# Performance work log

Hardware: AMD Instinct MI355X
Metric: run time of the kernel (lower is better)

Reference implementation:

```python
import jax, jax.numpy as jnp
import numpy as np

N = 50000
E = 1600000
F_IN = 256
DIMS = 64
N_CLS = 16
R = 8


def glorot(key, shape):
    fan = shape[-2] + shape[-1] if len(shape) >= 2 else shape[-1] * 2
    std = jnp.sqrt(6.0 / fan)
    return jax.random.uniform(key, shape, jnp.float32, -std, std)


def setup_inputs() -> dict:
    key = jax.random.key(0)
    ks = jax.random.split(key, 12)
    x = jax.random.normal(ks[0], (N, F_IN), jnp.float32)
    edge_index = jax.random.randint(ks[1], (2, E), 0, N)
    edge_weight = jax.random.uniform(ks[2], (E,), jnp.float32)
    edge_color = jax.random.randint(ks[3], (E,), 0, R)
    W1 = glorot(ks[4], (R, F_IN, DIMS))
    atten1 = glorot(ks[5], (R, 2 * DIMS))
    root1 = glorot(ks[6], (F_IN, DIMS))
    bias1 = jnp.zeros((DIMS,), jnp.float32)
    W2 = glorot(ks[7], (R, DIMS, N_CLS))
    atten2 = glorot(ks[8], (R, 2 * N_CLS))
    root2 = glorot(ks[9], (DIMS, N_CLS))
    bias2 = jnp.zeros((N_CLS,), jnp.float32)
    return dict(x=x, edge_index=edge_index, edge_weight=edge_weight,
                edge_color=edge_color, W1=W1, atten1=atten1, root1=root1,
                bias1=bias1, W2=W2, atten2=atten2, root2=root2, bias2=bias2)


def wrgat_conv(x, src, dst, ew, ec, W, atten, root, bias):
    # x: [N, f_in]; W: [R, f_in, d]; atten: [R, 2d]
    d = W.shape[-1]
    xr = jnp.einsum('nf,rfd->rnd', x, W)            # [R, N, d] per-relation projection
    xi = xr[ec, dst]                                 # [E, d] dst (x_i)
    xj = xr[ec, src]                                 # [E, d] src (x_j)
    a_i = atten[:, :d][ec]                           # [E, d]
    a_j = atten[:, d:][ec]
    s = jnp.sum(a_i * xi + a_j * xj, axis=-1)        # [E]
    s = jax.nn.leaky_relu(s, 0.2)
    # segment softmax over (relation, destination) groups
    seg = ec * N + dst                               # [E], each edge belongs to one relation
    nseg = R * N
    m = jax.ops.segment_max(s, seg, num_segments=nseg)
    m = jnp.where(jnp.isfinite(m), m, 0.0)           # empty segments -> 0
    e = jnp.exp(s - m[seg])
    denom = jax.ops.segment_sum(e, seg, num_segments=nseg)
    alpha = e / jnp.maximum(denom[seg], 1e-16)
    msg = (alpha * ew)[:, None] * xj                 # [E, d]
    summed = jax.ops.segment_sum(msg, seg, num_segments=nseg).reshape(R, N, d)
    cnt = jax.ops.segment_sum(jnp.ones_like(ew), seg, num_segments=nseg).reshape(R, N, 1)
    out = (summed / jnp.maximum(cnt, 1.0)).sum(axis=0)  # mean aggr per relation, summed over relations
    return out + x @ root + bias


def reference(x, edge_index, edge_weight, edge_color, W1, atten1, root1, bias1,
              W2, atten2, root2, bias2):
    src, dst = edge_index[0], edge_index[1]          # PyG flow source_to_target: x_j=src, x_i=dst
    h = wrgat_conv(x, src, dst, edge_weight, edge_color, W1, atten1, root1, bias1)
    h = jax.nn.relu(h)                               # dropout p=0 -> identity
    h = wrgat_conv(h, src, dst, edge_weight, edge_color, W2, atten2, root2, bias2)
    return jax.nn.log_softmax(h, axis=1)
```

## Files before the change

### kernel.cpp

```cpp
#include <hip/hip_runtime.h>
#include <math.h>

#define N_NODES 50000
#define N_EDGES 1600000
#define F_IN    256
#define DIMS    64
#define N_CLS   16
#define R_REL   8
#define CAP     96

#define PROJ_BLKS 3519
#define CSR_BLKS  6250
#define FRONT_BLKS (PROJ_BLKS + CSR_BLKS)

typedef short bf16x8 __attribute__((ext_vector_type(8)));
typedef float f32x4  __attribute__((ext_vector_type(4)));
typedef unsigned int u32;
typedef const __attribute__((address_space(1))) u32* gas_ptr;
typedef __attribute__((address_space(3))) u32* las_ptr;

__device__ __forceinline__ void async16(const void* g, void* l) {
    __builtin_amdgcn_global_load_lds((gas_ptr)g, (las_ptr)l, 16, 0, 0);
}

__device__ __forceinline__ unsigned short f2bf(float f) {
    unsigned u = __float_as_uint(f);
    unsigned r = (u + 0x7fffu + ((u >> 16) & 1u)) >> 16;
    return (unsigned short)r;
}
__device__ __forceinline__ float bf2f(unsigned short u) {
    return __uint_as_float(((unsigned)u) << 16);
}

__device__ __forceinline__ void csr_edge(
        int e, const int* __restrict__ ei, const int* __restrict__ ecol,
        const float* __restrict__ ew, int* __restrict__ fill,
        u32* __restrict__ rec) {
    int s = ei[e], d = ei[N_EDGES + e], c = ecol[e];
    float w_ = ew[e];
    int ewq = (int)(w_ * 4096.f);
    if (ewq > 4095) ewq = 4095;
    int p = atomicAdd(&fill[d], 1);
    int idx = (p < CAP) ? d * CAP + p : N_NODES * CAP;
    u32 rv = ((u32)c << 29) | ((u32)s << 12) | (u32)ewq;
    __builtin_nontemporal_store(rv, &rec[idx]);
}

__global__ __launch_bounds__(256) void cvt_x_kernel(
        const float* __restrict__ x, ushort* __restrict__ xb) {
    int i4 = blockIdx.x * 256 + threadIdx.x;
    float4 v = ((const float4*)x)[i4];
    ushort4 o;
    o.x = f2bf(v.x); o.y = f2bf(v.y); o.z = f2bf(v.z); o.w = f2bf(v.w);
    ((ushort4*)xb)[i4] = o;
}

__global__ __launch_bounds__(256) void cvt_w_kernel(
        const float* __restrict__ W1, const float* __restrict__ root1,
        ushort* __restrict__ wt1) {
    int idx = blockIdx.x * 256 + threadIdx.x;
    int r = idx >> 14, rem = idx & 16383;
    int n = rem >> 8, k = rem & 255;
    float v = (r < 8) ? W1[((size_t)r * F_IN + k) * DIMS + n]
                      : root1[(size_t)k * DIMS + n];
    wt1[idx] = f2bf(v);
}

#define BM 128
__global__ __launch_bounds__(256, 6) void front_kernel(
        const ushort* __restrict__ xb, const ushort* __restrict__ wt1,
        const float* __restrict__ at1,
        ushort* __restrict__ xr1b, ushort* __restrict__ hrootb,
        float* __restrict__ si1, float* __restrict__ sj1,
        const int* __restrict__ ei, const int* __restrict__ ecol,
        const float* __restrict__ ew, int* __restrict__ fill,
        u32* __restrict__ rec) {
    __shared__ ushort xs[BM * 64];
    const int bid = blockIdx.x;
    const int t = threadIdx.x;

    int pb = -1, cb = -1;
    if (bid < 2 * PROJ_BLKS) { if (bid & 1) cb = bid >> 1; else pb = bid >> 1; }
    else cb = PROJ_BLKS + (bid - 2 * PROJ_BLKS);

    if (cb >= 0) {
        csr_edge(cb * 256 + t, ei, ecol, ew, fill, rec);
        return;
    }

    const int r = pb / 391;
    const int node0 = (pb % 391) * BM;
    const ushort* wrow = wt1 + (size_t)r * 64 * 256;

    const int w = t >> 6, lane = t & 63;
    const int lane15 = lane & 15, quad = lane >> 4;
    const int row0 = w * 32 + lane15;
    const int sw0 = row0 & 7;

    f32x4 acc[2][4];
    #pragma unroll
    for (int a = 0; a < 2; ++a)
        #pragma unroll
        for (int b = 0; b < 4; ++b)
            acc[a][b] = (f32x4){0.f, 0.f, 0.f, 0.f};

    for (int s = 0; s < 4; ++s) {
        __syncthreads();
        #pragma unroll
        for (int c = 0; c < 4; ++c) {
            int slot = c * 256 + t;
            int row = slot >> 3, k8p = slot & 7;
            int k8 = k8p ^ (row & 7);
            int node = node0 + row;
            if (node >= N_NODES) node = N_NODES - 1;
            async16(&xb[(size_t)node * 256 + s * 64 + k8 * 8],
                    &xs[(c * 256 + w * 64) * 8]);
        }
        __syncthreads();
        #pragma unroll
        for (int kk = 0; kk < 2; ++kk) {
            int k8 = kk * 4 + quad;
            int aidx = row0 * 64 + ((k8 ^ sw0) << 3);
            bf16x8 a0 = *(const bf16x8*)&xs[aidx];
            bf16x8 a1 = *(const bf16x8*)&xs[aidx + 16 * 64];
            int kg = s * 64 + kk * 32 + quad * 8;
            #pragma unroll
            for (int nt = 0; nt < 4; ++nt) {
                bf16x8 b = *(const bf16x8*)&wrow[(size_t)(nt * 16 + lane15) * 256 + kg];
                acc[0][nt] = __builtin_amdgcn_mfma_f32_16x16x32_bf16(a0, b, acc[0][nt], 0, 0, 0);
                acc[1][nt] = __builtin_amdgcn_mfma_f32_16x16x32_bf16(a1, b, acc[1][nt], 0, 0, 0);
            }
        }
    }

    const float* at = at1 + r * 128;
    #pragma unroll
    for (int mt = 0; mt < 2; ++mt) {
        float pi[4] = {0.f, 0.f, 0.f, 0.f};
        float pj[4] = {0.f, 0.f, 0.f, 0.f};
        #pragma unroll
        for (int nt = 0; nt < 4; ++nt) {
            int gcol = nt * 16 + lane15;
            float ai = 0.f, aj = 0.f;
            if (r < 8) { ai = at[gcol]; aj = at[64 + gcol]; }
            #pragma unroll
            for (int reg = 0; reg < 4; ++reg) {
                float v = acc[mt][nt][reg];
                int grow = node0 + w * 32 + mt * 16 + quad * 4 + reg;
                if (grow < N_NODES) {
                    if (r < 8)
                        xr1b[((size_t)r * N_NODES + grow) * 64 + gcol] = f2bf(v);
                    else
                        hrootb[(size_t)grow * 64 + gcol] = f2bf(v);
                }
                pi[reg] += ai * v;
                pj[reg] += aj * v;
            }
        }
        if (r < 8) {
            #pragma unroll
            for (int reg = 0; reg < 4; ++reg) {
                float s_ = pi[reg], u_ = pj[reg];
                #pragma unroll
                for (int off = 1; off < 16; off <<= 1) {
                    s_ += __shfl_xor(s_, off, 64);
                    u_ += __shfl_xor(u_, off, 64);
                }
                if (lane15 == 0) {
                    int grow = node0 + w * 32 + mt * 16 + quad * 4 + reg;
                    if (grow < N_NODES) {
                        si1[r * N_NODES + grow] = s_;
                        sj1[r * N_NODES + grow] = u_;
                    }
                }
            }
        }
    }
}

__global__ __launch_bounds__(256) void agg1s_kernel(
        const u32* __restrict__ rec, const int* __restrict__ fill,
        const float* __restrict__ si, const float* __restrict__ sj,
        const ushort* __restrict__ xr1b, const ushort* __restrict__ hrootb,
        const float* __restrict__ bias1, ushort* __restrict__ hb,
        const float* __restrict__ W2, const float* __restrict__ at2,
        ushort* __restrict__ xr2b, float* __restrict__ si2,
        float* __restrict__ sj2) {
    __shared__ u32   esrc2[4][CAP];
    __shared__ float ecoef2[4][CAP];
    __shared__ float hval[4][64];
    __shared__ float sden[4][8];
    __shared__ int   scnt[4][8];
    __shared__ int   ccur[4][8];
    __shared__ float ssi[4][8];
    const int t = threadIdx.x;
    const int w = t >> 6, lane = t & 63;
    const int d = blockIdx.x * 4 + w;
    if (lane < 8) {
        sden[w][lane] = 0.f; scnt[w][lane] = 0;
        ssi[w][lane] = si[lane * N_NODES + d];
    }
    const int n = min(fill[d], CAP);
    const int base = d * CAP;
    u32 pv[2] = {0, 0};
    #pragma unroll
    for (int ii = 0; ii < 2; ++ii) {
        int i = lane + ii * 64;
        if (i < n) {
            u32 rv = rec[base + i];
            pv[ii] = rv;
            atomicAdd(&scnt[w][rv >> 29], 1);
        }
    }
    if (lane == 0) {
        int o = 0;
        #pragma unroll
        for (int c = 0; c < 8; ++c) { ccur[w][c] = o; o += scnt[w][c]; }
    }
    #pragma unroll
    for (int ii = 0; ii < 2; ++ii) {
        int i = lane + ii * 64;
        if (i < n) {
            int pos = atomicAdd(&ccur[w][pv[ii] >> 29], 1);
            esrc2[w][pos] = pv[ii];
        }
    }
    float exv[2] = {0.f, 0.f};
    #pragma unroll
    for (int ii = 0; ii < 2; ++ii) {
        int i = lane + ii * 64;
        if (i < n) {
            u32 rv = esrc2[w][i];
            int c = rv >> 29, s = (rv >> 12) & 0x1FFFF;
            float sc = ssi[w][c] + sj[c * N_NODES + s];
            sc = sc > 0.f ? sc : 0.2f * sc;
            float e = __expf(sc);
            exv[ii] = e;
            atomicAdd(&sden[w][c], e);
        }
    }
    #pragma unroll
    for (int ii = 0; ii < 2; ++ii) {
        int i = lane + ii * 64;
        if (i < n) {
            u32 rv = esrc2[w][i];
            int c = rv >> 29;
            float ewf = ((float)(rv & 0xFFF) + 0.5f) * (1.f / 4096.f);
            ecoef2[w][i] = exv[ii] / fmaxf(sden[w][c], 1e-16f)
                           * ewf / (float)scnt[w][c];
        }
    }
    float a0 = 0.f, a1 = 0.f, a2 = 0.f, a3 = 0.f;
    int i = 0;
    for (; i + 4 <= n; i += 4) {
        u32 p0 = esrc2[w][i],     p1 = esrc2[w][i + 1];
        u32 p2 = esrc2[w][i + 2], p3 = esrc2[w][i + 3];
        float c0 = ecoef2[w][i],     c1 = ecoef2[w][i + 1];
        float c2 = ecoef2[w][i + 2], c3 = ecoef2[w][i + 3];
        int r0 = (p0 >> 29) * N_NODES + ((p0 >> 12) & 0x1FFFF);
        int r1 = (p1 >> 29) * N_NODES + ((p1 >> 12) & 0x1FFFF);
        int r2 = (p2 >> 29) * N_NODES + ((p2 >> 12) & 0x1FFFF);
        int r3 = (p3 >> 29) * N_NODES + ((p3 >> 12) & 0x1FFFF);
        a0 += c0 * bf2f(xr1b[(size_t)r0 * 64 + lane]);
        a1 += c1 * bf2f(xr1b[(size_t)r1 * 64 + lane]);
        a2 += c2 * bf2f(xr1b[(size_t)r2 * 64 + lane]);
        a3 += c3 * bf2f(xr1b[(size_t)r3 * 64 + lane]);
    }
    for (; i < n; ++i) {
        u32 p0 = esrc2[w][i];
        int r0 = (p0 >> 29) * N_NODES + ((p0 >> 12) & 0x1FFFF);
        a0 += ecoef2[w][i] * bf2f(xr1b[(size_t)r0 * 64 + lane]);
    }
    float hf = (a0 + a1) + (a2 + a3)
               + bf2f(hrootb[(size_t)d * 64 + lane]) + bias1[lane];
    hf = fmaxf(hf, 0.f);
    hb[(size_t)d * 64 + lane] = f2bf(hf);
    hval[w][lane] = hf;
    const int r_ = lane >> 4, c_ = lane & 15;
    float v0 = 0.f, v1 = 0.f;
    #pragma unroll 8
    for (int k = 0; k < 64; ++k) {
        float hk = hval[w][k];
        v0 += hk * W2[((size_t)r_ * 64 + k) * 16 + c_];
        v1 += hk * W2[((size_t)(r_ + 4) * 64 + k) * 16 + c_];
    }
    xr2b[((size_t)r_ * N_NODES + d) * 16 + c_] = f2bf(v0);
    xr2b[((size_t)(r_ + 4) * N_NODES + d) * 16 + c_] = f2bf(v1);
    float s0 = at2[r_ * 32 + c_] * v0,        j0 = at2[r_ * 32 + 16 + c_] * v0;
    float s1 = at2[(r_ + 4) * 32 + c_] * v1,  j1 = at2[(r_ + 4) * 32 + 16 + c_] * v1;
    #pragma unroll
    for (int off = 1; off < 16; off <<= 1) {
        s0 += __shfl_xor(s0, off, 64); j0 += __shfl_xor(j0, off, 64);
        s1 += __shfl_xor(s1, off, 64); j1 += __shfl_xor(j1, off, 64);
    }
    if (c_ == 0) {
        si2[r_ * N_NODES + d] = s0;       sj2[r_ * N_NODES + d] = j0;
        si2[(r_ + 4) * N_NODES + d] = s1; sj2[(r_ + 4) * N_NODES + d] = j1;
    }
}

__global__ __launch_bounds__(256) void agg2s_kernel(
        const u32* __restrict__ rec, const int* __restrict__ fill,
        const float* __restrict__ si, const float* __restrict__ sj,
        const ushort* __restrict__ xr2b, const ushort* __restrict__ hb,
        const float* __restrict__ root2, const float* __restrict__ bias2,
        float* __restrict__ out) {
    __shared__ float rsh[64][17];
    __shared__ float hsh[4][64];
    __shared__ u32   esrc2[4][CAP];
    __shared__ float ecoef2[4][CAP];
    __shared__ float sden[4][8];
    __shared__ int   scnt[4][8];
    __shared__ int   ccur[4][8];
    __shared__ float ssi[4][8];
    const int t = threadIdx.x;
    for (int i = t; i < DIMS * N_CLS; i += 256) rsh[i >> 4][i & 15] = root2[i];
    const int w = t >> 6, lane = t & 63;
    const int d = blockIdx.x * 4 + w;
    hsh[w][lane] = bf2f(hb[(size_t)d * 64 + lane]);
    if (lane < 8) {
        sden[w][lane] = 0.f; scnt[w][lane] = 0;
        ssi[w][lane] = si[lane * N_NODES + d];
    }
    const int n = min(fill[d], CAP);
    const int base = d * CAP;
    u32 pv[2] = {0, 0};
    #pragma unroll
    for (int ii = 0; ii < 2; ++ii) {
        int i = lane + ii * 64;
        if (i < n) {
            u32 rv = rec[base + i];
            pv[ii] = rv;
            atomicAdd(&scnt[w][rv >> 29], 1);
        }
    }
    if (lane == 0) {
        int o = 0;
        #pragma unroll
        for (int c = 0; c < 8; ++c) { ccur[w][c] = o; o += scnt[w][c]; }
    }
    #pragma unroll
    for (int ii = 0; ii < 2; ++ii) {
        int i = lane + ii * 64;
        if (i < n) {
            int pos = atomicAdd(&ccur[w][pv[ii] >> 29], 1);
            esrc2[w][pos] = pv[ii];
        }
    }
    float exv[2] = {0.f, 0.f};
    #pragma unroll
    for (int ii = 0; ii < 2; ++ii) {
        int i = lane + ii * 64;
        if (i < n) {
            u32 rv = esrc2[w][i];
            int c = rv >> 29, s = (rv >> 12) & 0x1FFFF;
            float sc = ssi[w][c] + sj[c * N_NODES + s];
            sc = sc > 0.f ? sc : 0.2f * sc;
            float e = __expf(sc);
            exv[ii] = e;
            atomicAdd(&sden[w][c], e);
        }
    }
    #pragma unroll
    for (int ii = 0; ii < 2; ++ii) {
        int i = lane + ii * 64;
        if (i < n) {
            u32 rv = esrc2[w][i];
            int c = rv >> 29;
            float ewf = ((float)(rv & 0xFFF) + 0.5f) * (1.f / 4096.f);
            ecoef2[w][i] = exv[ii] / fmaxf(sden[w][c], 1e-16f)
                           * ewf / (float)scnt[w][c];
        }
    }
    __syncthreads();
    const int sub = lane >> 4, cd = lane & 15;
    float acc = 0.f;
    for (int i = sub; i < n; i += 4) {
        u32 p = esrc2[w][i];
        int row = (p >> 29) * N_NODES + ((p >> 12) & 0x1FFFF);
        acc += ecoef2[w][i] * bf2f(xr2b[(size_t)row * 16 + cd]);
    }
    #pragma unroll
    for (int k0 = 0; k0 < 16; ++k0) {
        int k = sub * 16 + k0;
        acc += hsh[w][k] * rsh[k][cd];
    }
    acc += __shfl_xor(acc, 16, 64);
    acc += __shfl_xor(acc, 32, 64);
    if (sub == 0) {
        acc += bias2[cd];
        float m = acc;
        #pragma unroll
        for (int off = 8; off; off >>= 1) m = fmaxf(m, __shfl_xor(m, off, 16));
        float ex2 = expf(acc - m);
        float ssum = ex2;
        #pragma unroll
        for (int off = 8; off; off >>= 1) ssum += __shfl_xor(ssum, off, 16);
        out[(size_t)d * 16 + cd] = acc - m - logf(ssum);
    }
}

extern "C" void kernel_launch(void* const* d_in, const int* in_sizes, int n_in,
                              void* d_out, int out_size, void* d_ws, size_t ws_size,
                              hipStream_t stream) {
    const float* x     = (const float*)d_in[0];
    const int*   ei    = (const int*)  d_in[1];
    const float* ew    = (const float*)d_in[2];
    const int*   ecol  = (const int*)  d_in[3];
    const float* W1    = (const float*)d_in[4];
    const float* at1   = (const float*)d_in[5];
    const float* root1 = (const float*)d_in[6];
    const float* b1    = (const float*)d_in[7];
    const float* W2    = (const float*)d_in[8];
    const float* at2   = (const float*)d_in[9];
    const float* root2 = (const float*)d_in[10];
    const float* b2    = (const float*)d_in[11];
    float* out = (float*)d_out;
    float* ws  = (float*)d_ws;

    ushort*   xb    = (ushort*)(ws + 0);
    ushort*   wt1   = (ushort*)(ws + 6400000);
    ushort*   xr1b  = (ushort*)(ws + 6480000);
    ushort*   hrootb= (ushort*)(ws + 19280000);
    ushort*   xr2b  = (ushort*)(ws + 20880000);
    float*    si1   = ws + 24080000;
    float*    sj1   = ws + 24480000;
    float*    si2   = ws + 24880000;
    float*    sj2   = ws + 25280000;
    int*      fill  = (int*)(ws + 25680000);
    ushort*   hb    = (ushort*)(ws + 25730000);
    u32*      rec   = (u32*)(ws + 27330000);

    hipMemsetAsync(fill, 0, (size_t)N_NODES * 4, stream);

    cvt_x_kernel<<<12500, 256, 0, stream>>>(x, xb);
    cvt_w_kernel<<<576, 256, 0, stream>>>(W1, root1, wt1);
    front_kernel<<<FRONT_BLKS, 256, 0, stream>>>(xb, wt1, at1, xr1b, hrootb,
                                                 si1, sj1, ei, ecol, ew, fill, rec);
    agg1s_kernel<<<12500, 256, 0, stream>>>(rec, fill, si1, sj1, xr1b, hrootb,
                                            b1, hb, W2, at2, xr2b, si2, sj2);
    agg2s_kernel<<<12500, 256, 0, stream>>>(rec, fill, si2, sj2, xr2b, hb,
                                            root2, b2, out);
}
```

Before: 434.3 us.

## Two-pass bucketed CSR build and split each node's aggregation across two waves

The per-edge global atomic on fill[d] is replaced with a two-pass build. First, edges are binned into 196 coarse destination buckets inside a fused x-conversion kernel. Then blocks in front_kernel scatter each bucket into per-node CSR slots using LDS atomics and write fill directly, which removes the fill memset. The aggregation kernels now process two nodes per block with two waves per node, splitting the edge gather loop and layer-2 projections between waves and combining partials through shared memory. This raises parallelism but adds block-wide syncs, an extra slab write/read of 8-byte records, and clamps overflow of bucket capacity.

```diff
diff --git a/kernel.cpp b/kernel.cpp
--- a/kernel.cpp
+++ b/kernel.cpp
@@ -8,14 +8,17 @@
 #define N_CLS   16
 #define R_REL   8
 #define CAP     96
+#define NBKT    196
+#define CAPB    9216
 
 #define PROJ_BLKS 3519
-#define CSR_BLKS  6250
-#define FRONT_BLKS (PROJ_BLKS + CSR_BLKS)
+#define CSRB_BLKS 392
+#define FRONT_BLKS (PROJ_BLKS + CSRB_BLKS)
 
 typedef short bf16x8 __attribute__((ext_vector_type(8)));
 typedef float f32x4  __attribute__((ext_vector_type(4)));
 typedef unsigned int u32;
+typedef unsigned long long u64;
 typedef const __attribute__((address_space(1))) u32* gas_ptr;
 typedef __attribute__((address_space(3))) u32* las_ptr;
 
@@ -32,27 +35,37 @@
     return __uint_as_float(((unsigned)u) << 16);
 }
 
-__device__ __forceinline__ void csr_edge(
-        int e, const int* __restrict__ ei, const int* __restrict__ ecol,
-        const float* __restrict__ ew, int* __restrict__ fill,
-        u32* __restrict__ rec) {
-    int s = ei[e], d = ei[N_EDGES + e], c = ecol[e];
-    float w_ = ew[e];
-    int ewq = (int)(w_ * 4096.f);
-    if (ewq > 4095) ewq = 4095;
-    int p = atomicAdd(&fill[d], 1);
-    int idx = (p < CAP) ? d * CAP + p : N_NODES * CAP;
-    u32 rv = ((u32)c << 29) | ((u32)s << 12) | (u32)ewq;
-    __builtin_nontemporal_store(rv, &rec[idx]);
-}
-
-__global__ __launch_bounds__(256) void cvt_x_kernel(
-        const float* __restrict__ x, ushort* __restrict__ xb) {
-    int i4 = blockIdx.x * 256 + threadIdx.x;
-    float4 v = ((const float4*)x)[i4];
-    ushort4 o;
-    o.x = f2bf(v.x); o.y = f2bf(v.y); o.z = f2bf(v.z); o.w = f2bf(v.w);
-    ((ushort4*)xb)[i4] = o;
+__global__ __launch_bounds__(256) void binx_kernel(
+        const float* __restrict__ x, ushort* __restrict__ xb,
+        const int* __restrict__ ei, const int* __restrict__ ecol,
+        const float* __restrict__ ew, int* __restrict__ bfill,
+        u64* __restrict__ slab) {
+    const int g = blockIdx.x / 17, m = blockIdx.x % 17;
+    const int t = threadIdx.x;
+    if (m < 16) {
+        int idx = g * 16 + m;
+        if (idx < 12500) {
+            int i4 = idx * 256 + t;
+            float4 v = ((const float4*)x)[i4];
+            ushort4 o;
+            o.x = f2bf(v.x); o.y = f2bf(v.y); o.z = f2bf(v.z); o.w = f2bf(v.w);
+            ((ushort4*)xb)[i4] = o;
+        }
+        return;
+    }
+    const int e0 = g * 2000;
+    for (int i = t; i < 2000; i += 256) {
+        int e = e0 + i;
+        int s = ei[e], d = ei[N_EDGES + e], c = ecol[e];
+        int ewq = (int)(ew[e] * 4096.f);
+        if (ewq > 4095) ewq = 4095;
+        int b = d >> 8;
+        int p = atomicAdd(&bfill[b], 1);
+        if (p >= CAPB) p = CAPB - 1;
+        u32 lo = ((u32)c << 29) | ((u32)s << 12) | (u32)ewq;
+        u64 rv = ((u64)(u32)d << 32) | lo;
+        __builtin_nontemporal_store(rv, &slab[(size_t)b * CAPB + p]);
+    }
 }
 
 __global__ __launch_bounds__(256) void cvt_w_kernel(
@@ -72,19 +85,37 @@
         const float* __restrict__ at1,
         ushort* __restrict__ xr1b, ushort* __restrict__ hrootb,
         float* __restrict__ si1, float* __restrict__ sj1,
-        const int* __restrict__ ei, const int* __restrict__ ecol,
-        const float* __restrict__ ew, int* __restrict__ fill,
-        u32* __restrict__ rec) {
+        const int* __restrict__ bfill, const u64* __restrict__ slab,
+        int* __restrict__ fill, u32* __restrict__ rec) {
     __shared__ ushort xs[BM * 64];
     const int bid = blockIdx.x;
     const int t = threadIdx.x;
 
     int pb = -1, cb = -1;
-    if (bid < 2 * PROJ_BLKS) { if (bid & 1) cb = bid >> 1; else pb = bid >> 1; }
-    else cb = PROJ_BLKS + (bid - 2 * PROJ_BLKS);
+    if (bid < 2 * CSRB_BLKS) { if (bid & 1) cb = bid >> 1; else pb = bid >> 1; }
+    else pb = CSRB_BLKS + (bid - 2 * CSRB_BLKS);
 
     if (cb >= 0) {
-        csr_edge(cb * 256 + t, ei, ecol, ew, fill, rec);
+        const int b = cb >> 1, half = cb & 1;
+        int* fl = (int*)xs;
+        if (t < 128) fl[t] = 0;
+        __syncthreads();
+        const int nb = min(bfill[b], CAPB);
+        const u64* sp = slab + (size_t)b * CAPB;
+        for (int i = t; i < nb; i += 256) {
+            u64 rv = sp[i];
+            int d = (int)(rv >> 32);
+            int dl = d & 255;
+            if ((dl >> 7) == half) {
+                int p = atomicAdd(&fl[dl & 127], 1);
+                if (p < CAP) rec[(size_t)d * CAP + p] = (u32)rv;
+            }
+        }
+        __syncthreads();
+        if (t < 128) {
+            int d = b * 256 + half * 128 + t;
+            if (d < N_NODES) fill[d] = fl[t];
+        }
         return;
     }
 
@@ -101,8 +132,8 @@
     #pragma unroll
     for (int a = 0; a < 2; ++a)
         #pragma unroll
-        for (int b = 0; b < 4; ++b)
-            acc[a][b] = (f32x4){0.f, 0.f, 0.f, 0.f};
+        for (int b_ = 0; b_ < 4; ++b_)
+            acc[a][b_] = (f32x4){0.f, 0.f, 0.f, 0.f};
 
     for (int s = 0; s < 4; ++s) {
         __syncthreads();
@@ -186,77 +217,70 @@
         const float* __restrict__ W2, const float* __restrict__ at2,
         ushort* __restrict__ xr2b, float* __restrict__ si2,
         float* __restrict__ sj2) {
-    __shared__ u32   esrc2[4][CAP];
-    __shared__ float ecoef2[4][CAP];
-    __shared__ float hval[4][64];
-    __shared__ float sden[4][8];
-    __shared__ int   scnt[4][8];
-    __shared__ int   ccur[4][8];
-    __shared__ float ssi[4][8];
+    __shared__ u32   esrc2[2][CAP];
+    __shared__ float ecoef2[2][CAP];
+    __shared__ float hval[2][64];
+    __shared__ float part[2][2][64];
+    __shared__ float sden[2][8];
+    __shared__ int   scnt[2][8];
+    __shared__ int   ccur[2][8];
+    __shared__ float ssi[2][8];
     const int t = threadIdx.x;
-    const int w = t >> 6, lane = t & 63;
-    const int d = blockIdx.x * 4 + w;
-    if (lane < 8) {
-        sden[w][lane] = 0.f; scnt[w][lane] = 0;
-        ssi[w][lane] = si[lane * N_NODES + d];
-    }
+    const int w2 = t >> 7;
+    const int sw = (t >> 6) & 1;
+    const int lane = t & 63;
+    const int d = blockIdx.x * 2 + w2;
+    if (sw == 0 && lane < 8) {
+        sden[w2][lane] = 0.f; scnt[w2][lane] = 0;
+        ssi[w2][lane] = si[lane * N_NODES + d];
+    }
+    __syncthreads();
     const int n = min(fill[d], CAP);
     const int base = d * CAP;
-    u32 pv[2] = {0, 0};
-    #pragma unroll
-    for (int ii = 0; ii < 2; ++ii) {
-        int i = lane + ii * 64;
-        if (i < n) {
-            u32 rv = rec[base + i];
-            pv[ii] = rv;
-            atomicAdd(&scnt[w][rv >> 29], 1);
-        }
-    }
-    if (lane == 0) {
+    const int i = sw * 64 + lane;
+    u32 pv = 0;
+    if (i < n) {
+        pv = rec[base + i];
+        atomicAdd(&scnt[w2][pv >> 29], 1);
+    }
+    __syncthreads();
+    if (sw == 0 && lane == 0) {
         int o = 0;
         #pragma unroll
-        for (int c = 0; c < 8; ++c) { ccur[w][c] = o; o += scnt[w][c]; }
-    }
-    #pragma unroll
-    for (int ii = 0; ii < 2; ++ii) {
-        int i = lane + ii * 64;
-        if (i < n) {
-            int pos = atomicAdd(&ccur[w][pv[ii] >> 29], 1);
-            esrc2[w][pos] = pv[ii];
-        }
-    }
-    float exv[2] = {0.f, 0.f};
-    #pragma unroll
-    for (int ii = 0; ii < 2; ++ii) {
-        int i = lane + ii * 64;
-        if (i < n) {
-            u32 rv = esrc2[w][i];
-            int c = rv >> 29, s = (rv >> 12) & 0x1FFFF;
-            float sc = ssi[w][c] + sj[c * N_NODES + s];
-            sc = sc > 0.f ? sc : 0.2f * sc;
-            float e = __expf(sc);
-            exv[ii] = e;
-            atomicAdd(&sden[w][c], e);
-        }
-    }
-    #pragma unroll
-    for (int ii = 0; ii < 2; ++ii) {
-        int i = lane + ii * 64;
-        if (i < n) {
-            u32 rv = esrc2[w][i];
-            int c = rv >> 29;
-            float ewf = ((float)(rv & 0xFFF) + 0.5f) * (1.f / 4096.f);
-            ecoef2[w][i] = exv[ii] / fmaxf(sden[w][c], 1e-16f)
-                           * ewf / (float)scnt[w][c];
-        }
-    }
+        for (int c = 0; c < 8; ++c) { ccur[w2][c] = o; o += scnt[w2][c]; }
+    }
+    __syncthreads();
+    if (i < n) {
+        int pos = atomicAdd(&ccur[w2][pv >> 29], 1);
+        esrc2[w2][pos] = pv;
+    }
+    __syncthreads();
+    float exv = 0.f;
+    u32 rv = 0;
+    if (i < n) {
+        rv = esrc2[w2][i];
+        int c = rv >> 29, s = (rv >> 12) & 0x1FFFF;
+        float sc = ssi[w2][c] + sj[c * N_NODES + s];
+        sc = sc > 0.f ? sc : 0.2f * sc;
+        exv = __expf(sc);
+        atomicAdd(&sden[w2][c], exv);
+    }
+    __syncthreads();
+    if (i < n) {
+        int c = rv >> 29;
+        float ewf = ((float)(rv & 0xFFF) + 0.5f) * (1.f / 4096.f);
+        ecoef2[w2][i] = exv / fmaxf(sden[w2][c], 1e-16f) * ewf / (float)scnt[w2][c];
+    }
+    __syncthreads();
+    const int nh = (n + 1) >> 1;
+    const int klo = sw * nh, khi = min(n, klo + nh);
     float a0 = 0.f, a1 = 0.f, a2 = 0.f, a3 = 0.f;
-    int i = 0;
-    for (; i + 4 <= n; i += 4) {
-        u32 p0 = esrc2[w][i],     p1 = esrc2[w][i + 1];
-        u32 p2 = esrc2[w][i + 2], p3 = esrc2[w][i + 3];
-        float c0 = ecoef2[w][i],     c1 = ecoef2[w][i + 1];
-        float c2 = ecoef2[w][i + 2], c3 = ecoef2[w][i + 3];
+    int k = klo;
+    for (; k + 4 <= khi; k += 4) {
+        u32 p0 = esrc2[w2][k],     p1 = esrc2[w2][k + 1];
+        u32 p2 = esrc2[w2][k + 2], p3 = esrc2[w2][k + 3];
+        float c0 = ecoef2[w2][k],     c1 = ecoef2[w2][k + 1];
+        float c2 = ecoef2[w2][k + 2], c3 = ecoef2[w2][k + 3];
         int r0 = (p0 >> 29) * N_NODES + ((p0 >> 12) & 0x1FFFF);
         int r1 = (p1 >> 29) * N_NODES + ((p1 >> 12) & 0x1FFFF);
         int r2 = (p2 >> 29) * N_NODES + ((p2 >> 12) & 0x1FFFF);
@@ -266,36 +290,36 @@
         a2 += c2 * bf2f(xr1b[(size_t)r2 * 64 + lane]);
         a3 += c3 * bf2f(xr1b[(size_t)r3 * 64 + lane]);
     }
-    for (; i < n; ++i) {
-        u32 p0 = esrc2[w][i];
+    for (; k < khi; ++k) {
+        u32 p0 = esrc2[w2][k];
         int r0 = (p0 >> 29) * N_NODES + ((p0 >> 12) & 0x1FFFF);
-        a0 += ecoef2[w][i] * bf2f(xr1b[(size_t)r0 * 64 + lane]);
-    }
-    float hf = (a0 + a1) + (a2 + a3)
-               + bf2f(hrootb[(size_t)d * 64 + lane]) + bias1[lane];
-    hf = fmaxf(hf, 0.f);
-    hb[(size_t)d * 64 + lane] = f2bf(hf);
-    hval[w][lane] = hf;
-    const int r_ = lane >> 4, c_ = lane & 15;
-    float v0 = 0.f, v1 = 0.f;
+        a0 += ecoef2[w2][k] * bf2f(xr1b[(size_t)r0 * 64 + lane]);
+    }
+    part[w2][sw][lane] = (a0 + a1) + (a2 + a3);
+    __syncthreads();
+    if (sw == 0) {
+        float hf = part[w2][0][lane] + part[w2][1][lane]
+                   + bf2f(hrootb[(size_t)d * 64 + lane]) + bias1[lane];
+        hf = fmaxf(hf, 0.f);
+        hb[(size_t)d * 64 + lane] = f2bf(hf);
+        hval[w2][lane] = hf;
+    }
+    __syncthreads();
+    const int r_ = (lane >> 4) + sw * 4, c_ = lane & 15;
+    float v0 = 0.f;
     #pragma unroll 8
-    for (int k = 0; k < 64; ++k) {
-        float hk = hval[w][k];
-        v0 += hk * W2[((size_t)r_ * 64 + k) * 16 + c_];
-        v1 += hk * W2[((size_t)(r_ + 4) * 64 + k) * 16 + c_];
-    }
+    for (int kk = 0; kk < 64; ++kk)
+        v0 += hval[w2][kk] * W2[((size_t)r_ * 64 + kk) * 16 + c_];
     xr2b[((size_t)r_ * N_NODES + d) * 16 + c_] = f2bf(v0);
-    xr2b[((size_t)(r_ + 4) * N_NODES + d) * 16 + c_] = f2bf(v1);
-    float s0 = at2[r_ * 32 + c_] * v0,        j0 = at2[r_ * 32 + 16 + c_] * v0;
-    float s1 = at2[(r_ + 4) * 32 + c_] * v1,  j1 = at2[(r_ + 4) * 32 + 16 + c_] * v1;
+    float s0 = at2[r_ * 32 + c_] * v0, j0 = at2[r_ * 32 + 16 + c_] * v0;
     #pragma unroll
     for (int off = 1; off < 16; off <<= 1) {
-        s0 += __shfl_xor(s0, off, 64); j0 += __shfl_xor(j0, off, 64);
-        s1 += __shfl_xor(s1, off, 64); j1 += __shfl_xor(j1, off, 64);
+        s0 += __shfl_xor(s0, off, 64);
+        j0 += __shfl_xor(j0, off, 64);
     }
     if (c_ == 0) {
-        si2[r_ * N_NODES + d] = s0;       sj2[r_ * N_NODES + d] = j0;
-        si2[(r_ + 4) * N_NODES + d] = s1; sj2[(r_ + 4) * N_NODES + d] = j1;
+        si2[r_ * N_NODES + d] = s0;
+        sj2[r_ * N_NODES + d] = j0;
     }
 }
 
@@ -306,97 +330,88 @@
         const float* __restrict__ root2, const float* __restrict__ bias2,
         float* __restrict__ out) {
     __shared__ float rsh[64][17];
-    __shared__ float hsh[4][64];
-    __shared__ u32   esrc2[4][CAP];
-    __shared__ float ecoef2[4][CAP];
-    __shared__ float sden[4][8];
-    __shared__ int   scnt[4][8];
-    __shared__ int   ccur[4][8];
-    __shared__ float ssi[4][8];
+    __shared__ float hsh[2][64];
+    __shared__ u32   esrc2[2][CAP];
+    __shared__ float ecoef2[2][CAP];
+    __shared__ float part[2][2][16];
+    __shared__ float sden[2][8];
+    __shared__ int   scnt[2][8];
+    __shared__ int   ccur[2][8];
+    __shared__ float ssi[2][8];
     const int t = threadIdx.x;
-    for (int i = t; i < DIMS * N_CLS; i += 256) rsh[i >> 4][i & 15] = root2[i];
-    const int w = t >> 6, lane = t & 63;
-    const int d = blockIdx.x * 4 + w;
-    hsh[w][lane] = bf2f(hb[(size_t)d * 64 + lane]);
-    if (lane < 8) {
-        sden[w][lane] = 0.f; scnt[w][lane] = 0;
-        ssi[w][lane] = si[lane * N_NODES + d];
-    }
+    for (int q = t; q < DIMS * N_CLS; q += 256) rsh[q >> 4][q & 15] = root2[q];
+    const int w2 = t >> 7, sw = (t >> 6) & 1, lane = t & 63;
+    const int d = blockIdx.x * 2 + w2;
+    if (sw == 0) hsh[w2][lane] = bf2f(hb[(size_t)d * 64 + lane]);
+    if (sw == 1 && lane < 8) {
+        sden[w2][lane] = 0.f; scnt[w2][lane] = 0;
+        ssi[w2][lane] = si[lane * N_NODES + d];
+    }
+    __syncthreads();
     const int n = min(fill[d], CAP);
     const int base = d * CAP;
-    u32 pv[2] = {0, 0};
+    const int i = sw * 64 + lane;
+    u32 pv = 0;
+    if (i < n) {
+        pv = rec[base + i];
+        atomicAdd(&scnt[w2][pv >> 29], 1);
+    }
+    __syncthreads();
+    if (sw == 0 && lane == 0) {
+        int o = 0;
+        #pragma unroll
+        for (int c = 0; c < 8; ++c) { ccur[w2][c] = o; o += scnt[w2][c]; }
+    }
+    __syncthreads();
+    if (i < n) {
+        int pos = atomicAdd(&ccur[w2][pv >> 29], 1);
+        esrc2[w2][pos] = pv;
+    }
+    __syncthreads();
+    float exv = 0.f;
+    u32 rv = 0;
+    if (i < n) {
+        rv = esrc2[w2][i];
+        int c = rv >> 29, s = (rv >> 12) & 0x1FFFF;
+        float sc = ssi[w2][c] + sj[c * N_NODES + s];
+        sc = sc > 0.f ? sc : 0.2f * sc;
+        exv = __expf(sc);
+        atomicAdd(&sden[w2][c], exv);
+    }
+    __syncthreads();
+    if (i < n) {
+        int c = rv >> 29;
+        float ewf = ((float)(rv & 0xFFF) + 0.5f) * (1.f / 4096.f);
+        ecoef2[w2][i] = exv / fmaxf(sden[w2][c], 1e-16f) * ewf / (float)scnt[w2][c];
+    }
+    __syncthreads();
+    const int sub = lane >> 4, cd = lane & 15;
+    const int j = sw * 4 + sub;
+    float acc = 0.f;
+    for (int k = j; k < n; k += 8) {
+        u32 p = esrc2[w2][k];
+        int row = (p >> 29) * N_NODES + ((p >> 12) & 0x1FFFF);
+        acc += ecoef2[w2][k] * bf2f(xr2b[(size_t)row * 16 + cd]);
+    }
     #pragma unroll
-    for (int ii = 0; ii < 2; ++ii) {
-        int i = lane + ii * 64;
-        if (i < n) {
-            u32 rv = rec[base + i];
-            pv[ii] = rv;
-            atomicAdd(&scnt[w][rv >> 29], 1);
-        }
-    }
-    if (lane == 0) {
-        int o = 0;
-        #pragma unroll
-        for (int c = 0; c < 8; ++c) { ccur[w][c] = o; o += scnt[w][c]; }
-    }
-    #pragma unroll
-    for (int ii = 0; ii < 2; ++ii) {
-        int i = lane + ii * 64;
-        if (i < n) {
-            int pos = atomicAdd(&ccur[w][pv[ii] >> 29], 1);
-            esrc2[w][pos] = pv[ii];
-        }
-    }
-    float exv[2] = {0.f, 0.f};
-    #pragma unroll
-    for (int ii = 0; ii < 2; ++ii) {
-        int i = lane + ii * 64;
-        if (i < n) {
-            u32 rv = esrc2[w][i];
-            int c = rv >> 29, s = (rv >> 12) & 0x1FFFF;
-            float sc = ssi[w][c] + sj[c * N_NODES + s];
-            sc = sc > 0.f ? sc : 0.2f * sc;
-            float e = __expf(sc);
-            exv[ii] = e;
-            atomicAdd(&sden[w][c], e);
-        }
-    }
-    #pragma unroll
-    for (int ii = 0; ii < 2; ++ii) {
-        int i = lane + ii * 64;
-        if (i < n) {
-            u32 rv = esrc2[w][i];
-            int c = rv >> 29;
-            float ewf = ((float)(rv & 0xFFF) + 0.5f) * (1.f / 4096.f);
-            ecoef2[w][i] = exv[ii] / fmaxf(sden[w][c], 1e-16f)
-                           * ewf / (float)scnt[w][c];
-        }
-    }
-    __syncthreads();
-    const int sub = lane >> 4, cd = lane & 15;
-    float acc = 0.f;
-    for (int i = sub; i < n; i += 4) {
-        u32 p = esrc2[w][i];
-        int row = (p >> 29) * N_NODES + ((p >> 12) & 0x1FFFF);
-        acc += ecoef2[w][i] * bf2f(xr2b[(size_t)row * 16 + cd]);
-    }
-    #pragma unroll
-    for (int k0 = 0; k0 < 16; ++k0) {
-        int k = sub * 16 + k0;
-        acc += hsh[w][k] * rsh[k][cd];
+    for (int k0 = 0; k0 < 8; ++k0) {
+        int kk = j * 8 + k0;
+        acc += hsh[w2][kk] * rsh[kk][cd];
     }
     acc += __shfl_xor(acc, 16, 64);
     acc += __shfl_xor(acc, 32, 64);
-    if (sub == 0) {
-        acc += bias2[cd];
-        float m = acc;
+    if (lane < 16) part[w2][sw][lane] = acc;
+    __syncthreads();
+    if (sw == 0 && lane < 16) {
+        float a = part[w2][0][lane] + part[w2][1][lane] + bias2[lane];
+        float m = a;
         #pragma unroll
         for (int off = 8; off; off >>= 1) m = fmaxf(m, __shfl_xor(m, off, 16));
-        float ex2 = expf(acc - m);
-        float ssum = ex2;
-        #pragma unroll
-        for (int off = 8; off; off >>= 1) ssum += __shfl_xor(ssum, off, 16);
-        out[(size_t)d * 16 + cd] = acc - m - logf(ssum);
+        float e = expf(a - m);
+        float ss = e;
+        #pragma unroll
+        for (int off = 8; off; off >>= 1) ss += __shfl_xor(ss, off, 16);
+        out[(size_t)d * 16 + lane] = a - m - logf(ss);
     }
 }
 
@@ -430,15 +445,17 @@
     int*      fill  = (int*)(ws + 25680000);
     ushort*   hb    = (ushort*)(ws + 25730000);
     u32*      rec   = (u32*)(ws + 27330000);
-
-    hipMemsetAsync(fill, 0, (size_t)N_NODES * 4, stream);
-
-    cvt_x_kernel<<<12500, 256, 0, stream>>>(x, xb);
+    u64*      slab  = (u64*)(ws + 32130000);
+    int*      bfill = (int*)(ws + 35742672);
+
+    hipMemsetAsync(bfill, 0, NBKT * 4, stream);
+
+    binx_kernel<<<13600, 256, 0, stream>>>(x, xb, ei, ecol, ew, bfill, slab);
     cvt_w_kernel<<<576, 256, 0, stream>>>(W1, root1, wt1);
     front_kernel<<<FRONT_BLKS, 256, 0, stream>>>(xb, wt1, at1, xr1b, hrootb,
-                                                 si1, sj1, ei, ecol, ew, fill, rec);
-    agg1s_kernel<<<12500, 256, 0, stream>>>(rec, fill, si1, sj1, xr1b, hrootb,
+                                                 si1, sj1, bfill, slab, fill, rec);
+    agg1s_kernel<<<25000, 256, 0, stream>>>(rec, fill, si1, sj1, xr1b, hrootb,
                                             b1, hb, W2, at2, xr2b, si2, sj2);
-    agg2s_kernel<<<12500, 256, 0, stream>>>(rec, fill, si2, sj2, xr2b, hb,
+    agg2s_kernel<<<25000, 256, 0, stream>>>(rec, fill, si2, sj2, xr2b, hb,
                                             root2, b2, out);
 }
```

New measurement: 1.308 ms. 3.01x slower.
